# Kernel tuning notes

Hardware: AMD Instinct MI355X
Metric: run time of the kernel (lower is better)

Reference implementation:

```python
import jax, jax.numpy as jnp
import numpy as np

N_NODES = 50000
N_EDGES = 800000
F_DIM = 128   # float_feat_dim
H_DIM = 64    # hidden_dim
NEG_SLOPE = 0.2


def setup_inputs() -> dict:
    key = jax.random.key(0)
    ks = jax.random.split(key, 12)
    in_dim = F_DIM + 1
    sc_in = 1.0 / np.sqrt(in_dim)
    sc_h = 1.0 / np.sqrt(H_DIM)
    return {
        "x_float": jax.random.normal(ks[0], (N_NODES, F_DIM), dtype=jnp.float32),
        "x_binary": jax.random.uniform(ks[1], (N_NODES,), dtype=jnp.float32),
        "edge_index": jax.random.randint(ks[2], (2, N_EDGES), 0, N_NODES, dtype=jnp.int64),
        "Wl": jax.random.normal(ks[3], (H_DIM, in_dim), dtype=jnp.float32) * sc_in,
        "bl": jnp.zeros((H_DIM,), dtype=jnp.float32),
        "Wr": jax.random.normal(ks[4], (H_DIM, in_dim), dtype=jnp.float32) * sc_in,
        "br": jnp.zeros((H_DIM,), dtype=jnp.float32),
        "att": jax.random.normal(ks[5], (H_DIM,), dtype=jnp.float32) * sc_h,
        "gat_bias": jnp.zeros((H_DIM,), dtype=jnp.float32),
        "Wo": jax.random.normal(ks[6], (F_DIM, H_DIM), dtype=jnp.float32) * sc_h,
        "bo": jnp.zeros((F_DIM,), dtype=jnp.float32),
        "dispersion": jnp.zeros((F_DIM,), dtype=jnp.float32),
    }


def reference(x_float, x_binary, edge_index, Wl, bl, Wr, br, att, gat_bias, Wo, bo, dispersion):
    N = x_float.shape[0]
    # concat float feats with binary feature -> [N, F+1]
    x = jnp.concatenate([x_float, x_binary[:, None]], axis=1)
    # add self loops (PyG GATv2Conv default)
    loops = jnp.arange(N, dtype=edge_index.dtype)
    src = jnp.concatenate([edge_index[0], loops])  # [E+N]
    dst = jnp.concatenate([edge_index[1], loops])
    # separate source/target linear projections (share_weights=False)
    xl = x @ Wl.T + bl  # [N, H]
    xr = x @ Wr.T + br  # [N, H]
    # per-edge GATv2 attention score: a^T LeakyReLU(x_l[j] + x_r[i])
    m = xl[src] + xr[dst]                      # [E+N, H]
    m = jnp.where(m > 0, m, NEG_SLOPE * m)
    e = m @ att                                # [E+N]
    # segment softmax over destination neighborhoods
    emax = jax.ops.segment_max(e, dst, num_segments=N)  # self loops => every seg nonempty
    ex = jnp.exp(e - emax[dst])
    denom = jax.ops.segment_sum(ex, dst, num_segments=N)
    alpha = ex / denom[dst]                    # [E+N]
    # weighted scatter-aggregate of source projections
    out = jax.ops.segment_sum(alpha[:, None] * xl[src], dst, num_segments=N) + gat_bias
    h = jax.nn.elu(out)                        # [N, H]
    logits = h @ Wo.T + bo                     # [N, F]
    return logits, jax.nn.softplus(dispersion)
```

## Files before the change

kernel.cpp:

```cpp
#include <hip/hip_runtime.h>
#include <hip/hip_bf16.h>
#include <math.h>

#define N_NODES 50000
#define N_EDGES 800000
#define F_DIM 128
#define H_DIM 64
#define IN_DIM 129
#define ETOT (N_EDGES + N_NODES)
#define PROJ_BLKS ((N_NODES + 31) / 32)
#define OUT_BLKS  ((N_NODES + 31) / 32)
#define NB 196
#define CAP 6144
#define EPB 3125
#define BKT_BLKS 256

typedef __hip_bfloat16 bf16;
typedef __attribute__((ext_vector_type(8))) short bf16x8;
typedef __attribute__((ext_vector_type(4))) float f32x4;

static __device__ __forceinline__ float bs2f(short s) {
    union { float f; unsigned u; } c; c.u = ((unsigned)(unsigned short)s) << 16; return c.f;
}
static __device__ __forceinline__ short f2bs(float f) {
    union { bf16 b; short s; } u; u.b = __float2bfloat16(f); return u.s;
}

__global__ __launch_bounds__(256) void prep_kernel(
    const float* __restrict__ Wl, const float* __restrict__ Wr,
    const float* __restrict__ Wo,
    bf16* __restrict__ whi, bf16* __restrict__ wlo,
    bf16* __restrict__ wohi, bf16* __restrict__ wolo,
    int* __restrict__ gtot)
{
    int b = blockIdx.x, t = threadIdx.x;
    if (b < 8) {
        int s = b * 256 + t;
        int fid = s >> 6, l = s & 63;
        int wave = fid >> 3, nt = (fid >> 2) & 1, ks = fid & 3;
        int ch = wave * 32 + nt * 16 + (l & 15);
        int kb = ks * 32 + (l >> 4) * 8;
        const float* wrow = (ch < 64) ? Wl + (size_t)ch * IN_DIM
                                      : Wr + (size_t)(ch - 64) * IN_DIM;
        #pragma unroll
        for (int j = 0; j < 8; ++j) {
            float v = wrow[kb + j];
            short hs = f2bs(v);
            short ls = f2bs(v - bs2f(hs));
            ((short*)whi)[(size_t)s * 8 + j] = hs;
            ((short*)wlo)[(size_t)s * 8 + j] = ls;
        }
    } else if (b < 12) {
        int s = (b - 8) * 256 + t;
        int fid = s >> 6, l = s & 63;
        int wave = fid >> 2, nt = (fid >> 1) & 1, ks = fid & 1;
        int ch = wave * 32 + nt * 16 + (l & 15);
        int kb = ks * 32 + (l >> 4) * 8;
        const float* wrow = Wo + (size_t)ch * H_DIM;
        #pragma unroll
        for (int j = 0; j < 8; ++j) {
            float v = wrow[kb + j];
            short hs = f2bs(v);
            short ls = f2bs(v - bs2f(hs));
            ((short*)wohi)[(size_t)s * 8 + j] = hs;
            ((short*)wolo)[(size_t)s * 8 + j] = ls;
        }
    } else {
        if (t < NB) gtot[t] = 0;
    }
}

__global__ __launch_bounds__(256) void h1_kernel(
    const float* __restrict__ xf, const float* __restrict__ xb,
    const float* __restrict__ Wl, const float* __restrict__ bl,
    const float* __restrict__ Wr, const float* __restrict__ br,
    const bf16* __restrict__ whi, const bf16* __restrict__ wlo,
    const int* __restrict__ esrc, const int* __restrict__ edst,
    bf16* __restrict__ xl, bf16* __restrict__ xr,
    int* __restrict__ gtot, unsigned* __restrict__ bstore2,
    int* __restrict__ bofsT)
{
    __shared__ int smem[2048];

    if (blockIdx.x >= PROJ_BLKS) {
        int* hist = smem;
        int* base = smem + 256;
        int* cur  = smem + 512;
        int* shs  = smem + 768;
        int t = threadIdx.x;
        int b = blockIdx.x - PROJ_BLKS;
        int e0 = b * EPB;
        if (t < NB) hist[t] = 0;
        __syncthreads();

        int myd[13]; int mys[13];
        #pragma unroll
        for (int i = 0; i < 13; ++i) {
            int k = t + i * 256;
            bool v = k < EPB;
            int dst = v ? edst[e0 + k] : -1;
            int sc  = v ? esrc[e0 + k] : 0;
            myd[i] = dst; mys[i] = sc;
            if (v) atomicAdd(&hist[dst >> 8], 1);
        }
        __syncthreads();

        int hv = (t < NB) ? hist[t] : 0;
        shs[t] = hv;
        __syncthreads();
        #pragma unroll
        for (int d = 1; d < 256; d <<= 1) {
            int x = (t >= d) ? shs[t - d] : 0;
            __syncthreads();
            shs[t] += x;
            __syncthreads();
        }
        if (t < NB) {
            int bs = shs[t] - hv;
            base[t] = bs;
            cur[t] = 0;
            if (hv) atomicAdd(&gtot[t], hv);
            bofsT[t * 256 + b] = (bs << 16) | hv;
        }
        __syncthreads();

        #pragma unroll
        for (int i = 0; i < 13; ++i) {
            if (myd[i] >= 0) {
                int j = myd[i] >> 8;
                int slot = base[j] + atomicAdd(&cur[j], 1);
                bstore2[(size_t)e0 + slot] =
                    ((unsigned)myd[i] << 16) | (unsigned)mys[i];
            }
        }
        return;
    }

    short* lds = (short*)smem;

    int wave = threadIdx.x >> 6;
    int lane = threadIdx.x & 63;
    int n = lane & 15, q = lane >> 4;
    int node0 = blockIdx.x * 32;

    bf16x8 bhi[2][4], blo_[2][4];
    float biasv[2], w128[2];
    #pragma unroll
    for (int nt = 0; nt < 2; ++nt) {
        int ch = wave * 32 + nt * 16 + n;
        #pragma unroll
        for (int ks = 0; ks < 4; ++ks) {
            int fid = wave * 8 + nt * 4 + ks;
            bhi[nt][ks]  = *(const bf16x8*)(whi + ((size_t)fid * 64 + lane) * 8);
            blo_[nt][ks] = *(const bf16x8*)(wlo + ((size_t)fid * 64 + lane) * 8);
        }
        biasv[nt] = (ch < 64) ? bl[ch] : br[ch - 64];
        w128[nt]  = (ch < 64) ? Wl[(size_t)ch * IN_DIM + 128]
                              : Wr[(size_t)(ch - 64) * IN_DIM + 128];
    }

    #pragma unroll
    for (int mt = 0; mt < 2; ++mt) {
        int nb = node0 + mt * 16;
        if (nb < N_NODES) {
            const float* xrow = xf + (size_t)(nb + n) * F_DIM;
            bf16x8 a[4];
            #pragma unroll
            for (int ks = 0; ks < 4; ++ks) {
                float4 u = *(const float4*)(xrow + ks * 32 + q * 8);
                float4 v = *(const float4*)(xrow + ks * 32 + q * 8 + 4);
                bf16x8 tt;
                tt[0] = f2bs(u.x); tt[1] = f2bs(u.y); tt[2] = f2bs(u.z); tt[3] = f2bs(u.w);
                tt[4] = f2bs(v.x); tt[5] = f2bs(v.y); tt[6] = f2bs(v.z); tt[7] = f2bs(v.w);
                a[ks] = tt;
            }
            f32x4 acc[2] = {{0.f,0.f,0.f,0.f},{0.f,0.f,0.f,0.f}};
            #pragma unroll
            for (int ks = 0; ks < 4; ++ks) {
                #pragma unroll
                for (int nt = 0; nt < 2; ++nt) {
                    acc[nt] = __builtin_amdgcn_mfma_f32_16x16x32_bf16(a[ks], bhi[nt][ks],  acc[nt], 0, 0, 0);
                    acc[nt] = __builtin_amdgcn_mfma_f32_16x16x32_bf16(a[ks], blo_[nt][ks], acc[nt], 0, 0, 0);
                }
            }
            float4 xbv = *(const float4*)(xb + nb + q * 4);
            float xbr[4] = {xbv.x, xbv.y, xbv.z, xbv.w};
            #pragma unroll
            for (int nt = 0; nt < 2; ++nt) {
                int ch = wave * 32 + nt * 16 + n;
                int blk = ch >> 3, pos = ch & 7;
                #pragma unroll
                for (int r = 0; r < 4; ++r) {
                    int nodeL = mt * 16 + q * 4 + r;
                    float val = acc[nt][r] + xbr[r] * w128[nt] + biasv[nt];
                    lds[nodeL * 128 + ((blk ^ (nodeL & 7)) << 3) + pos] = f2bs(val);
                }
            }
        }
    }
    __syncthreads();

    int nl = threadIdx.x >> 3, bk = threadIdx.x & 7;
    int node = node0 + nl;
    if (node < N_NODES) {
        bf16x8 v0 = *(const bf16x8*)(lds + nl * 128 + ((bk ^ (nl & 7)) << 3));
        *(bf16x8*)(xl + (size_t)node * H_DIM + bk * 8) = v0;
        bf16x8 v1 = *(const bf16x8*)(lds + nl * 128 + (((8 + bk) ^ (nl & 7)) << 3));
        *(bf16x8*)(xr + (size_t)node * H_DIM + bk * 8) = v1;
    }
}

__global__ __launch_bounds__(512) void csr_kernel(
    const int* __restrict__ gtot, const unsigned* __restrict__ bstore2,
    const int* __restrict__ bofsT,
    int* __restrict__ offs, int* __restrict__ csr_src)
{
    __shared__ unsigned ent[CAP];
    __shared__ int sh[256], gb_[256], bcnt_[256], bbase_[256];
    __shared__ int h256[256], start[256], c2[256];
    __shared__ int bb_s, C_s;
    int j = blockIdx.x, t = threadIdx.x;

    int bcnt = 0;
    if (t < 256) {
        unsigned v = (unsigned)bofsT[j * 256 + t];
        bbase_[t] = (int)(v >> 16);
        bcnt = (int)(v & 0xffffu);
        bcnt_[t] = bcnt;
        sh[t] = bcnt;
    }
    __syncthreads();
    #pragma unroll
    for (int d = 1; d < 256; d <<= 1) {
        int x = (t >= d && t < 256) ? sh[t - d] : 0;
        __syncthreads();
        if (t < 256) sh[t] += x;
        __syncthreads();
    }
    if (t < 256) gb_[t] = sh[t] - bcnt;
    if (t == 255) C_s = sh[255];
    __syncthreads();
    int C = C_s;

    if (t < 256) {
        const unsigned* p = bstore2 + (size_t)t * EPB + bbase_[t];
        int o = gb_[t];
        int c = bcnt_[t];
        for (int i = 0; i < c; ++i) ent[o + i] = p[i];
    }
    __syncthreads();

    int val = 0;
    if (t < NB) val = gtot[t] + ((t < NB - 1) ? 256 : (N_NODES - (NB - 1) * 256));
    if (t < 256) sh[t] = val;
    __syncthreads();
    #pragma unroll
    for (int d = 1; d < 256; d <<= 1) {
        int x = (t >= d && t < 256) ? sh[t - d] : 0;
        __syncthreads();
        if (t < 256) sh[t] += x;
        __syncthreads();
    }
    if (t == j) bb_s = sh[t] - val;
    if (t < 256) h256[t] = 0;
    __syncthreads();
    int bb = bb_s;

    for (int k = t; k < C; k += 512)
        atomicAdd(&h256[(ent[k] >> 16) & 255], 1);
    __syncthreads();

    int w = 0;
    if (t < 256) {
        w = h256[t] + ((j * 256 + t < N_NODES) ? 1 : 0);
        sh[t] = w;
    }
    __syncthreads();
    #pragma unroll
    for (int d = 1; d < 256; d <<= 1) {
        int x = (t >= d && t < 256) ? sh[t - d] : 0;
        __syncthreads();
        if (t < 256) sh[t] += x;
        __syncthreads();
    }
    if (t < 256) {
        int st = bb + sh[t] - w;
        start[t] = st;
        c2[t] = 0;
        int node = j * 256 + t;
        if (node < N_NODES) {
            offs[node] = st;
            csr_src[st] = node;
        }
    }
    if (j == NB - 1 && t == 0) offs[N_NODES] = ETOT;
    __syncthreads();

    for (int k = t; k < C; k += 512) {
        unsigned en = ent[k];
        int bin = (en >> 16) & 255;
        int r = atomicAdd(&c2[bin], 1);
        csr_src[start[bin] + 1 + r] = (int)(en & 0xffffu);
    }
}

__global__ __launch_bounds__(256) void agg_fused(
    const int* __restrict__ csr_src, const int* __restrict__ offs,
    const bf16* __restrict__ xl, const bf16* __restrict__ xr,
    const float* __restrict__ att, const float* __restrict__ gb,
    bf16* __restrict__ h)
{
    int wid  = (blockIdx.x * 256 + threadIdx.x) >> 6;
    int lane = threadIdx.x & 63;
    if (wid >= N_NODES) return;
    int g  = lane >> 3;
    int c8 = lane & 7;

    float attv[8], xrv[8];
    {
        bf16x8 xrow = *(const bf16x8*)(xr + (size_t)wid * H_DIM + c8 * 8);
        float4 a0 = *(const float4*)(att + c8 * 8);
        float4 a1 = *(const float4*)(att + c8 * 8 + 4);
        attv[0] = a0.x; attv[1] = a0.y; attv[2] = a0.z; attv[3] = a0.w;
        attv[4] = a1.x; attv[5] = a1.y; attv[6] = a1.z; attv[7] = a1.w;
        #pragma unroll
        for (int j = 0; j < 8; ++j) xrv[j] = bs2f(xrow[j]);
    }

    int beg = offs[wid];
    int end = offs[wid + 1];
    int last = end - 1;
    float den = 0.f;
    float acc[8] = {0.f, 0.f, 0.f, 0.f, 0.f, 0.f, 0.f, 0.f};

    int i0 = beg + g;        i0 = (i0 < end) ? i0 : last;
    int i1 = beg + 8 + g;    i1 = (i1 < end) ? i1 : last;
    int i2 = beg + 16 + g;   i2 = (i2 < end) ? i2 : last;
    int srcC = csr_src[i2];
    bf16x8 xa = *(const bf16x8*)(xl + (size_t)csr_src[i0] * H_DIM + c8 * 8);
    bf16x8 xb = *(const bf16x8*)(xl + (size_t)csr_src[i1] * H_DIM + c8 * 8);

    for (int base = beg; base < end; base += 8) {
        int i3 = base + 24 + g;  i3 = (i3 < end) ? i3 : last;
        int srcD = csr_src[i3];
        bf16x8 xc = *(const bf16x8*)(xl + (size_t)srcC * H_DIM + c8 * 8);

        bool valid = (base + g) < end;
        float xv[8], p = 0.f;
        #pragma unroll
        for (int j = 0; j < 8; ++j) {
            xv[j] = bs2f(xa[j]);
            float m = xv[j] + xrv[j];
            m = (m > 0.f) ? m : 0.2f * m;
            p += m * attv[j];
        }
        p += __shfl_xor(p, 1);
        p += __shfl_xor(p, 2);
        p += __shfl_xor(p, 4);
        float ex = valid ? __expf(p) : 0.f;
        den += ex;
        #pragma unroll
        for (int j = 0; j < 8; ++j) acc[j] += ex * xv[j];

        xa = xb;
        xb = xc;
        srcC = srcD;
    }

    #pragma unroll
    for (int j = 0; j < 8; ++j) {
        acc[j] += __shfl_xor(acc[j], 8);
        acc[j] += __shfl_xor(acc[j], 16);
        acc[j] += __shfl_xor(acc[j], 32);
    }
    den += __shfl_xor(den, 8);
    den += __shfl_xor(den, 16);
    den += __shfl_xor(den, 32);

    if (g == 0) {
        float inv = 1.0f / den;
        float4 g0 = *(const float4*)(gb + c8 * 8);
        float4 g1 = *(const float4*)(gb + c8 * 8 + 4);
        float gbv[8] = {g0.x, g0.y, g0.z, g0.w, g1.x, g1.y, g1.z, g1.w};
        bf16x8 ov;
        #pragma unroll
        for (int j = 0; j < 8; ++j) {
            float v = acc[j] * inv + gbv[j];
            v = (v > 0.f) ? v : expm1f(v);
            ov[j] = f2bs(v);
        }
        *(bf16x8*)(h + (size_t)wid * H_DIM + c8 * 8) = ov;
    }
}

__global__ __launch_bounds__(256) void out_mfma(
    const bf16* __restrict__ h,
    const bf16* __restrict__ wohi, const bf16* __restrict__ wolo,
    const float* __restrict__ bo, const float* __restrict__ disp,
    float* __restrict__ out)
{
    if (blockIdx.x == 0 && threadIdx.x < F_DIM) {
        float d = disp[threadIdx.x];
        out[(size_t)N_NODES * F_DIM + threadIdx.x] = (d > 20.f) ? d : log1pf(__expf(d));
    }

    __shared__ float ldso[32 * 132];

    int wave = threadIdx.x >> 6;
    int lane = threadIdx.x & 63;
    int n = lane & 15, q = lane >> 4;
    int node0 = blockIdx.x * 32;

    bf16x8 bhi[2][2], blo_[2][2];
    float bov[2];
    #pragma unroll
    for (int nt = 0; nt < 2; ++nt) {
        int ch = wave * 32 + nt * 16 + n;
        #pragma unroll
        for (int ks = 0; ks < 2; ++ks) {
            int fid = wave * 4 + nt * 2 + ks;
            bhi[nt][ks]  = *(const bf16x8*)(wohi + ((size_t)fid * 64 + lane) * 8);
            blo_[nt][ks] = *(const bf16x8*)(wolo + ((size_t)fid * 64 + lane) * 8);
        }
        bov[nt] = bo[ch];
    }

    #pragma unroll
    for (int mt = 0; mt < 2; ++mt) {
        int nb = node0 + mt * 16;
        if (nb < N_NODES) {
            const bf16* hrow = h + (size_t)(nb + n) * H_DIM;
            bf16x8 a[2];
            #pragma unroll
            for (int ks = 0; ks < 2; ++ks)
                a[ks] = *(const bf16x8*)(hrow + ks * 32 + q * 8);
            f32x4 acc[2] = {{0.f,0.f,0.f,0.f},{0.f,0.f,0.f,0.f}};
            #pragma unroll
            for (int ks = 0; ks < 2; ++ks) {
                #pragma unroll
                for (int nt = 0; nt < 2; ++nt) {
                    acc[nt] = __builtin_amdgcn_mfma_f32_16x16x32_bf16(a[ks], bhi[nt][ks],  acc[nt], 0, 0, 0);
                    acc[nt] = __builtin_amdgcn_mfma_f32_16x16x32_bf16(a[ks], blo_[nt][ks], acc[nt], 0, 0, 0);
                }
            }
            #pragma unroll
            for (int nt = 0; nt < 2; ++nt) {
                int ch = wave * 32 + nt * 16 + n;
                #pragma unroll
                for (int r = 0; r < 4; ++r) {
                    int nodeL = mt * 16 + q * 4 + r;
                    ldso[nodeL * 132 + ch] = acc[nt][r] + bov[nt];
                }
            }
        }
    }
    __syncthreads();

    int nl = threadIdx.x >> 3, c = threadIdx.x & 7;
    int node = node0 + nl;
    if (node < N_NODES) {
        const float* srcp = ldso + nl * 132 + c * 16;
        float* dstp = out + (size_t)node * F_DIM + c * 16;
        #pragma unroll
        for (int i = 0; i < 4; ++i)
            *(float4*)(dstp + i * 4) = *(const float4*)(srcp + i * 4);
    }
}

extern "C" void kernel_launch(void* const* d_in, const int* in_sizes, int n_in,
                              void* d_out, int out_size, void* d_ws, size_t ws_size,
                              hipStream_t stream)
{
    const float* xf  = (const float*)d_in[0];
    const float* xb  = (const float*)d_in[1];
    const int*   ei  = (const int*)d_in[2];
    const float* Wl  = (const float*)d_in[3];
    const float* bl  = (const float*)d_in[4];
    const float* Wr  = (const float*)d_in[5];
    const float* br  = (const float*)d_in[6];
    const float* att = (const float*)d_in[7];
    const float* gb  = (const float*)d_in[8];
    const float* Wo  = (const float*)d_in[9];
    const float* bo  = (const float*)d_in[10];
    const float* dp  = (const float*)d_in[11];
    float* out = (float*)d_out;
    const int* esrc = ei;
    const int* edst = ei + N_EDGES;

    char* ws = (char*)d_ws;
    const size_t SZB = (size_t)N_NODES * H_DIM * sizeof(bf16);
    bf16*  xl      = (bf16*)(ws);
    bf16*  xr      = (bf16*)(ws + SZB);
    bf16*  h       = (bf16*)(ws + 2 * SZB);
    unsigned* bstore2 = (unsigned*)h;
    int*   csr_src = (int*)(ws + 3 * SZB);
    int*   offs    = (int*)(ws + 3 * SZB + (size_t)ETOT * 4);
    int*   gtot    = offs + (N_NODES + 4);
    int*   bofsT   = gtot + 208;
    bf16*  whi     = (bf16*)(bofsT + NB * 256);
    bf16*  wlo     = whi + 16384;
    bf16*  wohi    = wlo + 16384;
    bf16*  wolo    = wohi + 8192;

    prep_kernel<<<13, 256, 0, stream>>>(Wl, Wr, Wo, whi, wlo, wohi, wolo, gtot);

    h1_kernel<<<PROJ_BLKS + BKT_BLKS, 256, 0, stream>>>(
        xf, xb, Wl, bl, Wr, br, whi, wlo, esrc, edst, xl, xr,
        gtot, bstore2, bofsT);

    csr_kernel<<<NB, 512, 0, stream>>>(gtot, bstore2, bofsT, offs, csr_src);

    agg_fused<<<(N_NODES * 64) / 256, 256, 0, stream>>>(csr_src, offs,
                                                        xl, xr, att, gb, h);

    out_mfma<<<OUT_BLKS, 256, 0, stream>>>(h, wohi, wolo, bo, dp, out);
}
```

Before: 186.0 us.

## Split fused projection/bucket kernel and deepen gather prefetch in aggregation

```diff
diff --git a/kernel.cpp b/kernel.cpp
--- a/kernel.cpp
+++ b/kernel.cpp
@@ -70,73 +70,72 @@
     }
 }
 
-__global__ __launch_bounds__(256) void h1_kernel(
+__global__ __launch_bounds__(256) void bucket_kernel(
+    const int* __restrict__ esrc, const int* __restrict__ edst,
+    int* __restrict__ gtot, unsigned* __restrict__ bstore2,
+    int* __restrict__ bofsT)
+{
+    __shared__ int smem[1024];
+    int* hist = smem;
+    int* base = smem + 256;
+    int* cur  = smem + 512;
+    int* shs  = smem + 768;
+    int t = threadIdx.x;
+    int b = blockIdx.x;
+    int e0 = b * EPB;
+    if (t < NB) hist[t] = 0;
+    __syncthreads();
+
+    int myd[13]; int mys[13];
+    #pragma unroll
+    for (int i = 0; i < 13; ++i) {
+        int k = t + i * 256;
+        bool v = k < EPB;
+        int dst = v ? edst[e0 + k] : -1;
+        int sc  = v ? esrc[e0 + k] : 0;
+        myd[i] = dst; mys[i] = sc;
+        if (v) atomicAdd(&hist[dst >> 8], 1);
+    }
+    __syncthreads();
+
+    int hv = (t < NB) ? hist[t] : 0;
+    shs[t] = hv;
+    __syncthreads();
+    #pragma unroll
+    for (int d = 1; d < 256; d <<= 1) {
+        int x = (t >= d) ? shs[t - d] : 0;
+        __syncthreads();
+        shs[t] += x;
+        __syncthreads();
+    }
+    if (t < NB) {
+        int bs = shs[t] - hv;
+        base[t] = bs;
+        cur[t] = 0;
+        if (hv) atomicAdd(&gtot[t], hv);
+        bofsT[t * 256 + b] = (bs << 16) | hv;
+    }
+    __syncthreads();
+
+    #pragma unroll
+    for (int i = 0; i < 13; ++i) {
+        if (myd[i] >= 0) {
+            int j = myd[i] >> 8;
+            int slot = base[j] + atomicAdd(&cur[j], 1);
+            bstore2[(size_t)e0 + slot] =
+                ((unsigned)myd[i] << 16) | (unsigned)mys[i];
+        }
+    }
+}
+
+__global__ __launch_bounds__(256) void proj_mfma(
     const float* __restrict__ xf, const float* __restrict__ xb,
     const float* __restrict__ Wl, const float* __restrict__ bl,
     const float* __restrict__ Wr, const float* __restrict__ br,
     const bf16* __restrict__ whi, const bf16* __restrict__ wlo,
-    const int* __restrict__ esrc, const int* __restrict__ edst,
-    bf16* __restrict__ xl, bf16* __restrict__ xr,
-    int* __restrict__ gtot, unsigned* __restrict__ bstore2,
-    int* __restrict__ bofsT)
-{
-    __shared__ int smem[2048];
-
-    if (blockIdx.x >= PROJ_BLKS) {
-        int* hist = smem;
-        int* base = smem + 256;
-        int* cur  = smem + 512;
-        int* shs  = smem + 768;
-        int t = threadIdx.x;
-        int b = blockIdx.x - PROJ_BLKS;
-        int e0 = b * EPB;
-        if (t < NB) hist[t] = 0;
-        __syncthreads();
-
-        int myd[13]; int mys[13];
-        #pragma unroll
-        for (int i = 0; i < 13; ++i) {
-            int k = t + i * 256;
-            bool v = k < EPB;
-            int dst = v ? edst[e0 + k] : -1;
-            int sc  = v ? esrc[e0 + k] : 0;
-            myd[i] = dst; mys[i] = sc;
-            if (v) atomicAdd(&hist[dst >> 8], 1);
-        }
-        __syncthreads();
-
-        int hv = (t < NB) ? hist[t] : 0;
-        shs[t] = hv;
-        __syncthreads();
-        #pragma unroll
-        for (int d = 1; d < 256; d <<= 1) {
-            int x = (t >= d) ? shs[t - d] : 0;
-            __syncthreads();
-            shs[t] += x;
-            __syncthreads();
-        }
-        if (t < NB) {
-            int bs = shs[t] - hv;
-            base[t] = bs;
-            cur[t] = 0;
-            if (hv) atomicAdd(&gtot[t], hv);
-            bofsT[t * 256 + b] = (bs << 16) | hv;
-        }
-        __syncthreads();
-
-        #pragma unroll
-        for (int i = 0; i < 13; ++i) {
-            if (myd[i] >= 0) {
-                int j = myd[i] >> 8;
-                int slot = base[j] + atomicAdd(&cur[j], 1);
-                bstore2[(size_t)e0 + slot] =
-                    ((unsigned)myd[i] << 16) | (unsigned)mys[i];
-            }
-        }
-        return;
-    }
-
-    short* lds = (short*)smem;
+    bf16* __restrict__ xl, bf16* __restrict__ xr)
+{
+    __shared__ short lds[32 * 128];
 
     int wave = threadIdx.x >> 6;
     int lane = threadIdx.x & 63;
@@ -330,26 +329,33 @@
     int beg = offs[wid];
     int end = offs[wid + 1];
     int last = end - 1;
+
+    #define CLMP(x) (((x) < end) ? (x) : last)
+
+    int j0 = csr_src[CLMP(beg + g)];
+    int j1 = csr_src[CLMP(beg + 8 + g)];
+    int j2 = csr_src[CLMP(beg + 16 + g)];
+    int j3 = csr_src[CLMP(beg + 24 + g)];
+    int s4 = csr_src[CLMP(beg + 32 + g)];
+    int s5 = csr_src[CLMP(beg + 40 + g)];
+    int s6 = csr_src[CLMP(beg + 48 + g)];
+    bf16x8 r0 = *(const bf16x8*)(xl + (size_t)j0 * H_DIM + c8 * 8);
+    bf16x8 r1 = *(const bf16x8*)(xl + (size_t)j1 * H_DIM + c8 * 8);
+    bf16x8 r2 = *(const bf16x8*)(xl + (size_t)j2 * H_DIM + c8 * 8);
+    bf16x8 r3 = *(const bf16x8*)(xl + (size_t)j3 * H_DIM + c8 * 8);
+
     float den = 0.f;
     float acc[8] = {0.f, 0.f, 0.f, 0.f, 0.f, 0.f, 0.f, 0.f};
 
-    int i0 = beg + g;        i0 = (i0 < end) ? i0 : last;
-    int i1 = beg + 8 + g;    i1 = (i1 < end) ? i1 : last;
-    int i2 = beg + 16 + g;   i2 = (i2 < end) ? i2 : last;
-    int srcC = csr_src[i2];
-    bf16x8 xa = *(const bf16x8*)(xl + (size_t)csr_src[i0] * H_DIM + c8 * 8);
-    bf16x8 xb = *(const bf16x8*)(xl + (size_t)csr_src[i1] * H_DIM + c8 * 8);
-
     for (int base = beg; base < end; base += 8) {
-        int i3 = base + 24 + g;  i3 = (i3 < end) ? i3 : last;
-        int srcD = csr_src[i3];
-        bf16x8 xc = *(const bf16x8*)(xl + (size_t)srcC * H_DIM + c8 * 8);
+        int s7 = csr_src[CLMP(base + 56 + g)];
+        bf16x8 r4 = *(const bf16x8*)(xl + (size_t)s4 * H_DIM + c8 * 8);
 
         bool valid = (base + g) < end;
         float xv[8], p = 0.f;
         #pragma unroll
         for (int j = 0; j < 8; ++j) {
-            xv[j] = bs2f(xa[j]);
+            xv[j] = bs2f(r0[j]);
             float m = xv[j] + xrv[j];
             m = (m > 0.f) ? m : 0.2f * m;
             p += m * attv[j];
@@ -362,10 +368,10 @@
         #pragma unroll
         for (int j = 0; j < 8; ++j) acc[j] += ex * xv[j];
 
-        xa = xb;
-        xb = xc;
-        srcC = srcD;
-    }
+        r0 = r1; r1 = r2; r2 = r3; r3 = r4;
+        s4 = s5; s5 = s6; s6 = s7;
+    }
+    #undef CLMP
 
     #pragma unroll
     for (int j = 0; j < 8; ++j) {
@@ -504,9 +510,10 @@
 
     prep_kernel<<<13, 256, 0, stream>>>(Wl, Wr, Wo, whi, wlo, wohi, wolo, gtot);
 
-    h1_kernel<<<PROJ_BLKS + BKT_BLKS, 256, 0, stream>>>(
-        xf, xb, Wl, bl, Wr, br, whi, wlo, esrc, edst, xl, xr,
-        gtot, bstore2, bofsT);
+    bucket_kernel<<<BKT_BLKS, 256, 0, stream>>>(esrc, edst, gtot, bstore2, bofsT);
+
+    proj_mfma<<<PROJ_BLKS, 256, 0, stream>>>(xf, xb, Wl, bl, Wr, br,
+                                             whi, wlo, xl, xr);
 
     csr_kernel<<<NB, 512, 0, stream>>>(gtot, bstore2, bofsT, offs, csr_src);
 
```

Result: slower. 195.6 us (+5.2%).

## Fuse GAT aggregation with output projection via shared-memory h tile

Applied to the files above, without the earlier changes.

```diff
diff --git a/kernel.cpp b/kernel.cpp
--- a/kernel.cpp
+++ b/kernel.cpp
@@ -9,11 +9,11 @@
 #define IN_DIM 129
 #define ETOT (N_EDGES + N_NODES)
 #define PROJ_BLKS ((N_NODES + 31) / 32)
-#define OUT_BLKS  ((N_NODES + 31) / 32)
 #define NB 196
 #define CAP 6144
 #define EPB 3125
 #define BKT_BLKS 256
+#define AGG_BLKS 3125
 
 typedef __hip_bfloat16 bf16;
 typedef __attribute__((ext_vector_type(8))) short bf16x8;
@@ -304,112 +304,117 @@
     }
 }
 
-__global__ __launch_bounds__(256) void agg_fused(
+__global__ __launch_bounds__(256) void agg_out(
     const int* __restrict__ csr_src, const int* __restrict__ offs,
     const bf16* __restrict__ xl, const bf16* __restrict__ xr,
     const float* __restrict__ att, const float* __restrict__ gb,
-    bf16* __restrict__ h)
+    const bf16* __restrict__ wohi, const bf16* __restrict__ wolo,
+    const float* __restrict__ bo, const float* __restrict__ disp,
+    float* __restrict__ out)
 {
-    int wid  = (blockIdx.x * 256 + threadIdx.x) >> 6;
+    __shared__ short hts[16 * 72];
+    __shared__ float ldso[16 * 132];
+
+    int wave = threadIdx.x >> 6;
     int lane = threadIdx.x & 63;
-    if (wid >= N_NODES) return;
     int g  = lane >> 3;
     int c8 = lane & 7;
-
-    float attv[8], xrv[8];
+    int node0 = blockIdx.x * 16;
+
+    if (blockIdx.x == 0 && threadIdx.x < F_DIM) {
+        float d = disp[threadIdx.x];
+        out[(size_t)N_NODES * F_DIM + threadIdx.x] = (d > 20.f) ? d : log1pf(__expf(d));
+    }
+
+    float attv[8], gbv[8];
     {
-        bf16x8 xrow = *(const bf16x8*)(xr + (size_t)wid * H_DIM + c8 * 8);
         float4 a0 = *(const float4*)(att + c8 * 8);
         float4 a1 = *(const float4*)(att + c8 * 8 + 4);
         attv[0] = a0.x; attv[1] = a0.y; attv[2] = a0.z; attv[3] = a0.w;
         attv[4] = a1.x; attv[5] = a1.y; attv[6] = a1.z; attv[7] = a1.w;
-        #pragma unroll
-        for (int j = 0; j < 8; ++j) xrv[j] = bs2f(xrow[j]);
-    }
-
-    int beg = offs[wid];
-    int end = offs[wid + 1];
-    int last = end - 1;
-    float den = 0.f;
-    float acc[8] = {0.f, 0.f, 0.f, 0.f, 0.f, 0.f, 0.f, 0.f};
-
-    int i0 = beg + g;        i0 = (i0 < end) ? i0 : last;
-    int i1 = beg + 8 + g;    i1 = (i1 < end) ? i1 : last;
-    int i2 = beg + 16 + g;   i2 = (i2 < end) ? i2 : last;
-    int srcC = csr_src[i2];
-    bf16x8 xa = *(const bf16x8*)(xl + (size_t)csr_src[i0] * H_DIM + c8 * 8);
-    bf16x8 xb = *(const bf16x8*)(xl + (size_t)csr_src[i1] * H_DIM + c8 * 8);
-
-    for (int base = beg; base < end; base += 8) {
-        int i3 = base + 24 + g;  i3 = (i3 < end) ? i3 : last;
-        int srcD = csr_src[i3];
-        bf16x8 xc = *(const bf16x8*)(xl + (size_t)srcC * H_DIM + c8 * 8);
-
-        bool valid = (base + g) < end;
-        float xv[8], p = 0.f;
-        #pragma unroll
-        for (int j = 0; j < 8; ++j) {
-            xv[j] = bs2f(xa[j]);
-            float m = xv[j] + xrv[j];
-            m = (m > 0.f) ? m : 0.2f * m;
-            p += m * attv[j];
-        }
-        p += __shfl_xor(p, 1);
-        p += __shfl_xor(p, 2);
-        p += __shfl_xor(p, 4);
-        float ex = valid ? __expf(p) : 0.f;
-        den += ex;
-        #pragma unroll
-        for (int j = 0; j < 8; ++j) acc[j] += ex * xv[j];
-
-        xa = xb;
-        xb = xc;
-        srcC = srcD;
-    }
-
-    #pragma unroll
-    for (int j = 0; j < 8; ++j) {
-        acc[j] += __shfl_xor(acc[j], 8);
-        acc[j] += __shfl_xor(acc[j], 16);
-        acc[j] += __shfl_xor(acc[j], 32);
-    }
-    den += __shfl_xor(den, 8);
-    den += __shfl_xor(den, 16);
-    den += __shfl_xor(den, 32);
-
-    if (g == 0) {
-        float inv = 1.0f / den;
         float4 g0 = *(const float4*)(gb + c8 * 8);
         float4 g1 = *(const float4*)(gb + c8 * 8 + 4);
-        float gbv[8] = {g0.x, g0.y, g0.z, g0.w, g1.x, g1.y, g1.z, g1.w};
-        bf16x8 ov;
+        gbv[0] = g0.x; gbv[1] = g0.y; gbv[2] = g0.z; gbv[3] = g0.w;
+        gbv[4] = g1.x; gbv[5] = g1.y; gbv[6] = g1.z; gbv[7] = g1.w;
+    }
+
+    #pragma unroll 1
+    for (int i = 0; i < 4; ++i) {
+        int wd  = wave * 4 + i;
+        int wid = node0 + wd;
+
+        float xrv[8];
+        {
+            bf16x8 xrow = *(const bf16x8*)(xr + (size_t)wid * H_DIM + c8 * 8);
+            #pragma unroll
+            for (int j = 0; j < 8; ++j) xrv[j] = bs2f(xrow[j]);
+        }
+
+        int beg = offs[wid];
+        int end = offs[wid + 1];
+        int last = end - 1;
+        float den = 0.f;
+        float acc[8] = {0.f, 0.f, 0.f, 0.f, 0.f, 0.f, 0.f, 0.f};
+
+        int i0 = beg + g;        i0 = (i0 < end) ? i0 : last;
+        int i1 = beg + 8 + g;    i1 = (i1 < end) ? i1 : last;
+        int i2 = beg + 16 + g;   i2 = (i2 < end) ? i2 : last;
+        int srcC = csr_src[i2];
+        bf16x8 xa = *(const bf16x8*)(xl + (size_t)csr_src[i0] * H_DIM + c8 * 8);
+        bf16x8 xb = *(const bf16x8*)(xl + (size_t)csr_src[i1] * H_DIM + c8 * 8);
+
+        for (int base = beg; base < end; base += 8) {
+            int i3 = base + 24 + g;  i3 = (i3 < end) ? i3 : last;
+            int srcD = csr_src[i3];
+            bf16x8 xc = *(const bf16x8*)(xl + (size_t)srcC * H_DIM + c8 * 8);
+
+            bool valid = (base + g) < end;
+            float xv[8], p = 0.f;
+            #pragma unroll
+            for (int j = 0; j < 8; ++j) {
+                xv[j] = bs2f(xa[j]);
+                float m = xv[j] + xrv[j];
+                m = (m > 0.f) ? m : 0.2f * m;
+                p += m * attv[j];
+            }
+            p += __shfl_xor(p, 1);
+            p += __shfl_xor(p, 2);
+            p += __shfl_xor(p, 4);
+            float ex = valid ? __expf(p) : 0.f;
+            den += ex;
+            #pragma unroll
+            for (int j = 0; j < 8; ++j) acc[j] += ex * xv[j];
+
+            xa = xb;
+            xb = xc;
+            srcC = srcD;
+        }
+
         #pragma unroll
         for (int j = 0; j < 8; ++j) {
-            float v = acc[j] * inv + gbv[j];
-            v = (v > 0.f) ? v : expm1f(v);
-            ov[j] = f2bs(v);
-        }
-        *(bf16x8*)(h + (size_t)wid * H_DIM + c8 * 8) = ov;
-    }
-}
-
-__global__ __launch_bounds__(256) void out_mfma(
-    const bf16* __restrict__ h,
-    const bf16* __restrict__ wohi, const bf16* __restrict__ wolo,
-    const float* __restrict__ bo, const float* __restrict__ disp,
-    float* __restrict__ out)
-{
-    if (blockIdx.x == 0 && threadIdx.x < F_DIM) {
-        float d = disp[threadIdx.x];
-        out[(size_t)N_NODES * F_DIM + threadIdx.x] = (d > 20.f) ? d : log1pf(__expf(d));
-    }
-
-    __shared__ float ldso[32 * 132];
-
-    int wave = threadIdx.x >> 6;
-    int lane = threadIdx.x & 63;
+            acc[j] += __shfl_xor(acc[j], 8);
+            acc[j] += __shfl_xor(acc[j], 16);
+            acc[j] += __shfl_xor(acc[j], 32);
+        }
+        den += __shfl_xor(den, 8);
+        den += __shfl_xor(den, 16);
+        den += __shfl_xor(den, 32);
+
+        if (g == 0) {
+            float inv = 1.0f / den;
+            bf16x8 ov;
+            #pragma unroll
+            for (int j = 0; j < 8; ++j) {
+                float v = acc[j] * inv + gbv[j];
+                v = (v > 0.f) ? v : expm1f(v);
+                ov[j] = f2bs(v);
+            }
+            *(bf16x8*)(hts + wd * 72 + c8 * 8) = ov;
+        }
+    }
+    __syncthreads();
+
     int n = lane & 15, q = lane >> 4;
-    int node0 = blockIdx.x * 32;
 
     bf16x8 bhi[2][2], blo_[2][2];
     float bov[2];
@@ -425,46 +430,35 @@
         bov[nt] = bo[ch];
     }
 
-    #pragma unroll
-    for (int mt = 0; mt < 2; ++mt) {
-        int nb = node0 + mt * 16;
-        if (nb < N_NODES) {
-            const bf16* hrow = h + (size_t)(nb + n) * H_DIM;
-            bf16x8 a[2];
-            #pragma unroll
-            for (int ks = 0; ks < 2; ++ks)
-                a[ks] = *(const bf16x8*)(hrow + ks * 32 + q * 8);
-            f32x4 acc[2] = {{0.f,0.f,0.f,0.f},{0.f,0.f,0.f,0.f}};
-            #pragma unroll
-            for (int ks = 0; ks < 2; ++ks) {
-                #pragma unroll
-                for (int nt = 0; nt < 2; ++nt) {
-                    acc[nt] = __builtin_amdgcn_mfma_f32_16x16x32_bf16(a[ks], bhi[nt][ks],  acc[nt], 0, 0, 0);
-                    acc[nt] = __builtin_amdgcn_mfma_f32_16x16x32_bf16(a[ks], blo_[nt][ks], acc[nt], 0, 0, 0);
-                }
-            }
-            #pragma unroll
-            for (int nt = 0; nt < 2; ++nt) {
-                int ch = wave * 32 + nt * 16 + n;
-                #pragma unroll
-                for (int r = 0; r < 4; ++r) {
-                    int nodeL = mt * 16 + q * 4 + r;
-                    ldso[nodeL * 132 + ch] = acc[nt][r] + bov[nt];
-                }
-            }
-        }
-    }
-    __syncthreads();
-
-    int nl = threadIdx.x >> 3, c = threadIdx.x & 7;
-    int node = node0 + nl;
-    if (node < N_NODES) {
-        const float* srcp = ldso + nl * 132 + c * 16;
-        float* dstp = out + (size_t)node * F_DIM + c * 16;
-        #pragma unroll
-        for (int i = 0; i < 4; ++i)
-            *(float4*)(dstp + i * 4) = *(const float4*)(srcp + i * 4);
-    }
+    bf16x8 a[2];
+    #pragma unroll
+    for (int ks = 0; ks < 2; ++ks)
+        a[ks] = *(const bf16x8*)(hts + n * 72 + ks * 32 + q * 8);
+    f32x4 acc2[2] = {{0.f,0.f,0.f,0.f},{0.f,0.f,0.f,0.f}};
+    #pragma unroll
+    for (int ks = 0; ks < 2; ++ks) {
+        #pragma unroll
+        for (int nt = 0; nt < 2; ++nt) {
+            acc2[nt] = __builtin_amdgcn_mfma_f32_16x16x32_bf16(a[ks], bhi[nt][ks],  acc2[nt], 0, 0, 0);
+            acc2[nt] = __builtin_amdgcn_mfma_f32_16x16x32_bf16(a[ks], blo_[nt][ks], acc2[nt], 0, 0, 0);
+        }
+    }
+    #pragma unroll
+    for (int nt = 0; nt < 2; ++nt) {
+        int ch = wave * 32 + nt * 16 + n;
+        #pragma unroll
+        for (int r = 0; r < 4; ++r) {
+            int nodeL = q * 4 + r;
+            ldso[nodeL * 132 + ch] = acc2[nt][r] + bov[nt];
+        }
+    }
+    __syncthreads();
+
+    int nl = threadIdx.x >> 4, p = threadIdx.x & 15;
+    const float* srcp = ldso + nl * 132 + p * 8;
+    float* dstp = out + (size_t)(node0 + nl) * F_DIM + p * 8;
+    *(float4*)(dstp)     = *(const float4*)(srcp);
+    *(float4*)(dstp + 4) = *(const float4*)(srcp + 4);
 }
 
 extern "C" void kernel_launch(void* const* d_in, const int* in_sizes, int n_in,
@@ -491,10 +485,9 @@
     const size_t SZB = (size_t)N_NODES * H_DIM * sizeof(bf16);
     bf16*  xl      = (bf16*)(ws);
     bf16*  xr      = (bf16*)(ws + SZB);
-    bf16*  h       = (bf16*)(ws + 2 * SZB);
-    unsigned* bstore2 = (unsigned*)h;
-    int*   csr_src = (int*)(ws + 3 * SZB);
-    int*   offs    = (int*)(ws + 3 * SZB + (size_t)ETOT * 4);
+    unsigned* bstore2 = (unsigned*)(ws + 2 * SZB);
+    int*   csr_src = (int*)(ws + 2 * SZB + (size_t)N_EDGES * 4);
+    int*   offs    = csr_src + ETOT;
     int*   gtot    = offs + (N_NODES + 4);
     int*   bofsT   = gtot + 208;
     bf16*  whi     = (bf16*)(bofsT + NB * 256);
@@ -510,8 +503,6 @@
 
     csr_kernel<<<NB, 512, 0, stream>>>(gtot, bstore2, bofsT, offs, csr_src);
 
-    agg_fused<<<(N_NODES * 64) / 256, 256, 0, stream>>>(csr_src, offs,
-                                                        xl, xr, att, gb, h);
-
-    out_mfma<<<OUT_BLKS, 256, 0, stream>>>(h, wohi, wolo, bo, dp, out);
-}
+    agg_out<<<AGG_BLKS, 256, 0, stream>>>(csr_src, offs, xl, xr, att, gb,
+                                          wohi, wolo, bo, dp, out);
+}
```

After: 187.2 us. No clear change (+0.7%).
